# Performance work log

Measured on AMD Instinct MI355X. Metric: run time of the kernel, lower is better.

## Reference

```python
import jax, jax.numpy as jnp
import numpy as np

# DCT-III (a.k.a. IDCT), unnormalized, scaled to match the DREAMPlace kernel:
#   y_k = x_0 + 2 * sum_{n=1}^{N-1} x_n * cos(pi * n * (2k+1) / (2N))
# (the docstring's Re{1/2 x0 + sum xn e^{j pi n (2k+1)/(2N)}} scaled by 2).
# Computed in O(N log N) via a length-2N FFT:
#   y_k = Re{ sum_n c_n x_n e^{j pi n/(2N)} e^{2 pi j n k/(2N)} }
# which is 2N * ifft(pad(a, 2N)) evaluated at k = 0..N-1, with
#   a_n = c_n * x_n * exp(j pi n / (2N)),  c_0 = 1, c_{n>0} = 2.

def _idct_last_dim(x):
    N = x.shape[-1]
    n = jnp.arange(N)
    c = jnp.where(n == 0, 1.0, 2.0).astype(x.dtype)
    twiddle = jnp.exp(1j * (jnp.pi / (2 * N)) * n.astype(jnp.float32)).astype(jnp.complex64)
    a = (c * x).astype(jnp.complex64) * twiddle          # [.., N]
    y = jnp.fft.ifft(a, n=2 * N, axis=-1)                # [.., 2N]
    return (y.real[..., :N] * (2 * N)).astype(x.dtype)


def setup_inputs() -> dict:
    key = jax.random.key(0)
    x = jax.random.normal(key, (4096, 4096), dtype=jnp.float32)
    return {"x": x}


def reference(x) -> jnp.ndarray:
    return _idct_last_dim(x)
```

## Files before the change

kernel.cpp:

```cpp
#include <hip/hip_runtime.h>
#include <cstdint>


#define NN 4096
#define HH 2048
#define BM 128
#define BN 128
#define BK 128

typedef int i32x4 __attribute__((ext_vector_type(4)));
typedef int i32x2 __attribute__((ext_vector_type(2)));

__device__ __forceinline__ void async_copy16(void* lds_base, const void* gptr) {
    __builtin_amdgcn_global_load_lds(
        (const __attribute__((address_space(1))) unsigned int*)gptr,
        (__attribute__((address_space(3))) unsigned int*)lds_base,
        16, 0, 0);
}

__device__ __forceinline__ int pack4(int q0, int q1, int q2, int q3) {
    return (q0 & 255) | ((q1 & 255) << 8) | ((q2 & 255) << 16) | ((q3 & 255) << 24);
}

__global__ __launch_bounds__(256) void prep_i8(const float* __restrict__ x,
                                               signed char* __restrict__ Ae,
                                               signed char* __restrict__ Ao,
                                               signed char* __restrict__ CEm,
                                               signed char* __restrict__ COm,
                                               float* __restrict__ se,
                                               float* __restrict__ so) {
    const int b = blockIdx.x;
    const int t = threadIdx.x;
    const float s = 3.834951969714103e-4f;

    if (b < 4096) {
        __shared__ float wmaxe[4], wmaxo[4];
        const float* xr = x + (size_t)b * NN;
        float v[16];
#pragma unroll
        for (int j = 0; j < 4; ++j) {
            float4 f = ((const float4*)xr)[t * 4 + j];
            v[j * 4 + 0] = f.x; v[j * 4 + 1] = f.y;
            v[j * 4 + 2] = f.z; v[j * 4 + 3] = f.w;
        }
        float emax = 1e-30f, omax = 1e-30f;
#pragma unroll
        for (int i = 0; i < 8; ++i) {
            emax = fmaxf(emax, __builtin_fabsf(v[2 * i]));
            omax = fmaxf(omax, __builtin_fabsf(v[2 * i + 1]));
        }
#pragma unroll
        for (int m = 1; m < 64; m <<= 1) {
            emax = fmaxf(emax, __shfl_xor(emax, m));
            omax = fmaxf(omax, __shfl_xor(omax, m));
        }
        const int wv = t >> 6;
        if ((t & 63) == 0) { wmaxe[wv] = emax; wmaxo[wv] = omax; }
        __syncthreads();
        const float rmax_e = fmaxf(fmaxf(wmaxe[0], wmaxe[1]), fmaxf(wmaxe[2], wmaxe[3]));
        const float rmax_o = fmaxf(fmaxf(wmaxo[0], wmaxo[1]), fmaxf(wmaxo[2], wmaxo[3]));
        const float inv_e = 127.0f / rmax_e, inv_o = 127.0f / rmax_o;
        int qe[8], qo[8];
#pragma unroll
        for (int i = 0; i < 8; ++i) {
            qe[i] = (int)rintf(v[2 * i] * inv_e);
            qo[i] = (int)rintf(v[2 * i + 1] * inv_o);
        }
        i32x2 oe, oo;
        oe[0] = pack4(qe[0], qe[1], qe[2], qe[3]);
        oe[1] = pack4(qe[4], qe[5], qe[6], qe[7]);
        oo[0] = pack4(qo[0], qo[1], qo[2], qo[3]);
        oo[1] = pack4(qo[4], qo[5], qo[6], qo[7]);
        ((i32x2*)(Ae + (size_t)b * HH))[t] = oe;
        ((i32x2*)(Ao + (size_t)b * HH))[t] = oo;
        if (t == 0) {
            se[b] = rmax_e * (1.0f / 127.0f);
            so[b] = rmax_o * (1.0f / 127.0f);
        }
    } else if (b < 6144) {
        const int k = b - 4096;
        const int twok1 = 2 * k + 1;
        int q[8];
#pragma unroll
        for (int i = 0; i < 8; ++i) {
            int m = t * 8 + i;
            int p = (2 * m * twok1) & 16383;
            float w = (m == 0) ? 1.0f : 2.0f;
            q[i] = (int)rintf(w * __cosf((float)p * s) * 63.5f);
        }
        i32x2 o;
        o[0] = pack4(q[0], q[1], q[2], q[3]);
        o[1] = pack4(q[4], q[5], q[6], q[7]);
        ((i32x2*)(CEm + (size_t)k * HH))[t] = o;
    } else {
        const int k = b - 6144;
        const int twok1 = 2 * k + 1;
        int q[8];
#pragma unroll
        for (int i = 0; i < 8; ++i) {
            int m = t * 8 + i;
            int p = ((2 * m + 1) * twok1) & 16383;
            q[i] = (int)rintf(__cosf((float)p * s) * 127.0f);
        }
        i32x2 o;
        o[0] = pack4(q[0], q[1], q[2], q[3]);
        o[1] = pack4(q[4], q[5], q[6], q[7]);
        ((i32x2*)(COm + (size_t)k * HH))[t] = o;
    }
}

__global__ __launch_bounds__(256, 2) void idct_gemm2(const signed char* __restrict__ Ae,
                                                     const signed char* __restrict__ Ao,
                                                     const signed char* __restrict__ CEm,
                                                     const signed char* __restrict__ COm,
                                                     const float* __restrict__ se,
                                                     const float* __restrict__ so,
                                                     float* __restrict__ C) {
    __shared__ __align__(16) signed char sAe[BM * BK];
    __shared__ __align__(16) signed char sAo[BM * BK];
    __shared__ __align__(16) signed char sCE[BN * BK];
    __shared__ __align__(16) signed char sCO[BN * BK];

    const int tid  = threadIdx.x;
    const int wave = tid >> 6;
    const int lane = tid & 63;
    const int waveM = wave >> 1;
    const int waveN = wave & 1;

    const int rowBase = blockIdx.y * BM;
    const int colBase = blockIdx.x * BN;

    i32x4 accE[4][4] = {};
    i32x4 accO[4][4] = {};

    const int srow  = lane >> 3;
    const int sgran = lane & 7;
    const int ggcol = (sgran ^ srow) * 16;
    const int rmod  = lane & 7;
    const int quad  = lane >> 4;

    for (int k0 = 0; k0 < HH; k0 += BK) {
#pragma unroll
        for (int j = 0; j < 4; ++j) {
            int ck = wave * 4 + j;
            int r  = ck * 8 + srow;
            size_t aoff = (size_t)(rowBase + r) * HH + k0 + ggcol;
            size_t boff = (size_t)(colBase + r) * HH + k0 + ggcol;
            async_copy16(&sAe[ck * 1024], Ae + aoff);
            async_copy16(&sAo[ck * 1024], Ao + aoff);
            async_copy16(&sCE[ck * 1024], CEm + boff);
            async_copy16(&sCO[ck * 1024], COm + boff);
        }
        __syncthreads();

#pragma unroll
        for (int kk = 0; kk < 2; ++kk) {
            const int poff = ((kk * 4 + quad) ^ rmod) * 16;
            {
                i32x4 af[4], bfr[4];
#pragma unroll
                for (int mi = 0; mi < 4; ++mi) {
                    int r = waveM * 64 + mi * 16 + (lane & 15);
                    af[mi] = *(const i32x4*)&sAe[r * BK + poff];
                }
#pragma unroll
                for (int ni = 0; ni < 4; ++ni) {
                    int r = waveN * 64 + ni * 16 + (lane & 15);
                    bfr[ni] = *(const i32x4*)&sCE[r * BK + poff];
                }
#pragma unroll
                for (int mi = 0; mi < 4; ++mi)
#pragma unroll
                    for (int ni = 0; ni < 4; ++ni)
                        accE[mi][ni] = __builtin_amdgcn_mfma_i32_16x16x64_i8(
                            af[mi], bfr[ni], accE[mi][ni], 0, 0, 0);
            }
            {
                i32x4 af[4], bfr[4];
#pragma unroll
                for (int mi = 0; mi < 4; ++mi) {
                    int r = waveM * 64 + mi * 16 + (lane & 15);
                    af[mi] = *(const i32x4*)&sAo[r * BK + poff];
                }
#pragma unroll
                for (int ni = 0; ni < 4; ++ni) {
                    int r = waveN * 64 + ni * 16 + (lane & 15);
                    bfr[ni] = *(const i32x4*)&sCO[r * BK + poff];
                }
#pragma unroll
                for (int mi = 0; mi < 4; ++mi)
#pragma unroll
                    for (int ni = 0; ni < 4; ++ni)
                        accO[mi][ni] = __builtin_amdgcn_mfma_i32_16x16x64_i8(
                            af[mi], bfr[ni], accO[mi][ni], 0, 0, 0);
            }
        }
        __syncthreads();
    }

    const float sB_s = 2.0f / 127.0f;
    const int mrow0 = rowBase + waveM * 64 + (lane >> 4) * 4;
    const int ncol0 = colBase + waveN * 64 + (lane & 15);
#pragma unroll
    for (int mi = 0; mi < 4; ++mi)
#pragma unroll
        for (int ni = 0; ni < 4; ++ni)
#pragma unroll
            for (int rg = 0; rg < 4; ++rg) {
                int rr = mrow0 + mi * 16 + rg;
                int cc = ncol0 + ni * 16;
                float e = (float)accE[mi][ni][rg] * (se[rr] * sB_s);
                float o = (float)accO[mi][ni][rg] * (so[rr] * sB_s);
                C[(size_t)rr * NN + cc] = e + o;
                C[(size_t)rr * NN + (NN - 1 - cc)] = e - o;
            }
}

__global__ __launch_bounds__(256) void idct_naive(const float* __restrict__ x,
                                                  float* __restrict__ out) {
    int row = blockIdx.x;
    __shared__ float sx[NN];
    for (int i = threadIdx.x; i < NN; i += 256) sx[i] = x[(size_t)row * NN + i];
    __syncthreads();
    const float s = 3.834951969714103e-4f;
    for (int k = threadIdx.x; k < NN; k += 256) {
        int twok1 = 2 * k + 1;
        float acc = sx[0];
        int p = 0;
        for (int n = 1; n < NN; ++n) {
            p += twok1; p &= 16383;
            acc += 2.0f * sx[n] * __cosf((float)p * s);
        }
        out[(size_t)row * NN + k] = acc;
    }
}

extern "C" void kernel_launch(void* const* d_in, const int* in_sizes, int n_in,
                              void* d_out, int out_size, void* d_ws, size_t ws_size,
                              hipStream_t stream) {
    const float* x = (const float*)d_in[0];
    float* out = (float*)d_out;

    const size_t eA = (size_t)NN * HH;
    const size_t eC = (size_t)HH * HH;
    const size_t need = 2 * eA + 2 * eC + 2 * NN * sizeof(float);

    if (ws_size >= need) {
        signed char* Ae = (signed char*)d_ws;
        signed char* Ao = Ae + eA;
        signed char* CEm = Ao + eA;
        signed char* COm = CEm + eC;
        float* se = (float*)(COm + eC);
        float* so = se + NN;

        prep_i8<<<8192, 256, 0, stream>>>(x, Ae, Ao, CEm, COm, se, so);

        dim3 grid(HH / BN, NN / BM);
        idct_gemm2<<<grid, 256, 0, stream>>>(Ae, Ao, CEm, COm, se, so, out);
    } else {
        idct_naive<<<NN, 256, 0, stream>>>(x, out);
    }
}
```

Baseline: 146.0 us.

## Double-buffer LDS tiles in int8 IDCT GEMM with 512-thread blocks

Converts the int8 MFMA GEMM main loop to a double-buffered LDS pipeline: the next K-tile is issued with async global-to-LDS copies while the current tile is computed. The block grows to 8 waves, each owning a 64x32 output sub-tile, and MFMA sections are wrapped in s_setprio raises. This is meant to hide global load latency behind matrix math. The cost is that LDS per block doubles to 128KB, which likely limits occupancy to one block per CU, and each wave gets less register reuse per fragment load.

```diff
diff --git a/kernel.cpp b/kernel.cpp
--- a/kernel.cpp
+++ b/kernel.cpp
@@ -7,6 +7,7 @@
 #define BM 128
 #define BN 128
 #define BK 128
+#define NT (HH / BK)
 
 typedef int i32x4 __attribute__((ext_vector_type(4)));
 typedef int i32x2 __attribute__((ext_vector_type(2)));
@@ -109,102 +110,116 @@
     }
 }
 
-__global__ __launch_bounds__(256, 2) void idct_gemm2(const signed char* __restrict__ Ae,
+__global__ __launch_bounds__(512, 2) void idct_gemm2(const signed char* __restrict__ Ae,
                                                      const signed char* __restrict__ Ao,
                                                      const signed char* __restrict__ CEm,
                                                      const signed char* __restrict__ COm,
                                                      const float* __restrict__ se,
                                                      const float* __restrict__ so,
                                                      float* __restrict__ C) {
-    __shared__ __align__(16) signed char sAe[BM * BK];
-    __shared__ __align__(16) signed char sAo[BM * BK];
-    __shared__ __align__(16) signed char sCE[BN * BK];
-    __shared__ __align__(16) signed char sCO[BN * BK];
+    __shared__ __align__(16) signed char sAe[2][BM * BK];
+    __shared__ __align__(16) signed char sAo[2][BM * BK];
+    __shared__ __align__(16) signed char sCE[2][BN * BK];
+    __shared__ __align__(16) signed char sCO[2][BN * BK];
 
     const int tid  = threadIdx.x;
     const int wave = tid >> 6;
     const int lane = tid & 63;
-    const int waveM = wave >> 1;
-    const int waveN = wave & 1;
+    const int waveM = wave >> 2;
+    const int waveN = wave & 3;
 
     const int rowBase = blockIdx.y * BM;
     const int colBase = blockIdx.x * BN;
 
-    i32x4 accE[4][4] = {};
-    i32x4 accO[4][4] = {};
+    i32x4 accE[4][2] = {};
+    i32x4 accO[4][2] = {};
 
     const int srow  = lane >> 3;
     const int sgran = lane & 7;
     const int ggcol = (sgran ^ srow) * 16;
     const int rmod  = lane & 7;
     const int quad  = lane >> 4;
-
-    for (int k0 = 0; k0 < HH; k0 += BK) {
-#pragma unroll
-        for (int j = 0; j < 4; ++j) {
-            int ck = wave * 4 + j;
-            int r  = ck * 8 + srow;
-            size_t aoff = (size_t)(rowBase + r) * HH + k0 + ggcol;
-            size_t boff = (size_t)(colBase + r) * HH + k0 + ggcol;
-            async_copy16(&sAe[ck * 1024], Ae + aoff);
-            async_copy16(&sAo[ck * 1024], Ao + aoff);
-            async_copy16(&sCE[ck * 1024], CEm + boff);
-            async_copy16(&sCO[ck * 1024], COm + boff);
-        }
-        __syncthreads();
-
-#pragma unroll
-        for (int kk = 0; kk < 2; ++kk) {
-            const int poff = ((kk * 4 + quad) ^ rmod) * 16;
-            {
-                i32x4 af[4], bfr[4];
-#pragma unroll
-                for (int mi = 0; mi < 4; ++mi) {
-                    int r = waveM * 64 + mi * 16 + (lane & 15);
-                    af[mi] = *(const i32x4*)&sAe[r * BK + poff];
-                }
-#pragma unroll
-                for (int ni = 0; ni < 4; ++ni) {
-                    int r = waveN * 64 + ni * 16 + (lane & 15);
-                    bfr[ni] = *(const i32x4*)&sCE[r * BK + poff];
-                }
-#pragma unroll
-                for (int mi = 0; mi < 4; ++mi)
-#pragma unroll
-                    for (int ni = 0; ni < 4; ++ni)
-                        accE[mi][ni] = __builtin_amdgcn_mfma_i32_16x16x64_i8(
-                            af[mi], bfr[ni], accE[mi][ni], 0, 0, 0);
-            }
-            {
-                i32x4 af[4], bfr[4];
-#pragma unroll
-                for (int mi = 0; mi < 4; ++mi) {
-                    int r = waveM * 64 + mi * 16 + (lane & 15);
-                    af[mi] = *(const i32x4*)&sAo[r * BK + poff];
-                }
-#pragma unroll
-                for (int ni = 0; ni < 4; ++ni) {
-                    int r = waveN * 64 + ni * 16 + (lane & 15);
-                    bfr[ni] = *(const i32x4*)&sCO[r * BK + poff];
-                }
-#pragma unroll
-                for (int mi = 0; mi < 4; ++mi)
-#pragma unroll
-                    for (int ni = 0; ni < 4; ++ni)
-                        accO[mi][ni] = __builtin_amdgcn_mfma_i32_16x16x64_i8(
-                            af[mi], bfr[ni], accO[mi][ni], 0, 0, 0);
-            }
-        }
-        __syncthreads();
-    }
+    const int ck0   = wave * 2;
+
+    const size_t aRow = (size_t)(rowBase + ck0 * 8 + srow) * HH + ggcol;
+    const size_t bRow = (size_t)(colBase + ck0 * 8 + srow) * HH + ggcol;
+
+#define STAGE(BUF, K0)                                                        \
+    do {                                                                      \
+        _Pragma("unroll")                                                     \
+        for (int j = 0; j < 2; ++j) {                                         \
+            size_t aoff = aRow + (size_t)j * 8 * HH + (size_t)(K0);           \
+            size_t boff = bRow + (size_t)j * 8 * HH + (size_t)(K0);           \
+            async_copy16(&sAe[BUF][(ck0 + j) * 1024], Ae + aoff);             \
+            async_copy16(&sAo[BUF][(ck0 + j) * 1024], Ao + aoff);             \
+            async_copy16(&sCE[BUF][(ck0 + j) * 1024], CEm + boff);            \
+            async_copy16(&sCO[BUF][(ck0 + j) * 1024], COm + boff);            \
+        }                                                                     \
+    } while (0)
+
+#define COMPUTE(BUF)                                                          \
+    do {                                                                      \
+        _Pragma("unroll")                                                     \
+        for (int kk = 0; kk < 2; ++kk) {                                      \
+            const int poff = ((kk * 4 + quad) ^ rmod) * 16;                   \
+            i32x4 af[4], bfr[2];                                              \
+            _Pragma("unroll")                                                 \
+            for (int mi = 0; mi < 4; ++mi)                                    \
+                af[mi] = *(const i32x4*)&sAe[BUF][(waveM * 64 + mi * 16 + (lane & 15)) * BK + poff]; \
+            _Pragma("unroll")                                                 \
+            for (int ni = 0; ni < 2; ++ni)                                    \
+                bfr[ni] = *(const i32x4*)&sCE[BUF][(waveN * 32 + ni * 16 + (lane & 15)) * BK + poff]; \
+            __builtin_amdgcn_s_setprio(1);                                    \
+            _Pragma("unroll")                                                 \
+            for (int mi = 0; mi < 4; ++mi)                                    \
+                _Pragma("unroll")                                             \
+                for (int ni = 0; ni < 2; ++ni)                                \
+                    accE[mi][ni] = __builtin_amdgcn_mfma_i32_16x16x64_i8(     \
+                        af[mi], bfr[ni], accE[mi][ni], 0, 0, 0);              \
+            __builtin_amdgcn_s_setprio(0);                                    \
+            _Pragma("unroll")                                                 \
+            for (int mi = 0; mi < 4; ++mi)                                    \
+                af[mi] = *(const i32x4*)&sAo[BUF][(waveM * 64 + mi * 16 + (lane & 15)) * BK + poff]; \
+            _Pragma("unroll")                                                 \
+            for (int ni = 0; ni < 2; ++ni)                                    \
+                bfr[ni] = *(const i32x4*)&sCO[BUF][(waveN * 32 + ni * 16 + (lane & 15)) * BK + poff]; \
+            __builtin_amdgcn_s_setprio(1);                                    \
+            _Pragma("unroll")                                                 \
+            for (int mi = 0; mi < 4; ++mi)                                    \
+                _Pragma("unroll")                                             \
+                for (int ni = 0; ni < 2; ++ni)                                \
+                    accO[mi][ni] = __builtin_amdgcn_mfma_i32_16x16x64_i8(     \
+                        af[mi], bfr[ni], accO[mi][ni], 0, 0, 0);              \
+            __builtin_amdgcn_s_setprio(0);                                    \
+        }                                                                     \
+    } while (0)
+
+    STAGE(0, 0);
+    asm volatile("s_waitcnt vmcnt(0)" ::: "memory");
+    __builtin_amdgcn_s_barrier();
+
+#pragma unroll 1
+    for (int t = 0; t < NT; t += 2) {
+        STAGE(1, (t + 1) * BK);
+        COMPUTE(0);
+        asm volatile("s_waitcnt vmcnt(0) lgkmcnt(0)" ::: "memory");
+        __builtin_amdgcn_s_barrier();
+
+        if (t + 2 < NT) STAGE(0, (t + 2) * BK);
+        COMPUTE(1);
+        asm volatile("s_waitcnt vmcnt(0) lgkmcnt(0)" ::: "memory");
+        __builtin_amdgcn_s_barrier();
+    }
+#undef STAGE
+#undef COMPUTE
 
     const float sB_s = 2.0f / 127.0f;
     const int mrow0 = rowBase + waveM * 64 + (lane >> 4) * 4;
-    const int ncol0 = colBase + waveN * 64 + (lane & 15);
+    const int ncol0 = colBase + waveN * 32 + (lane & 15);
 #pragma unroll
     for (int mi = 0; mi < 4; ++mi)
 #pragma unroll
-        for (int ni = 0; ni < 4; ++ni)
+        for (int ni = 0; ni < 2; ++ni)
 #pragma unroll
             for (int rg = 0; rg < 4; ++rg) {
                 int rr = mrow0 + mi * 16 + rg;
@@ -256,7 +271,7 @@
         prep_i8<<<8192, 256, 0, stream>>>(x, Ae, Ao, CEm, COm, se, so);
 
         dim3 grid(HH / BN, NN / BM);
-        idct_gemm2<<<grid, 256, 0, stream>>>(Ae, Ao, CEm, COm, se, so, out);
+        idct_gemm2<<<grid, 512, 0, stream>>>(Ae, Ao, CEm, COm, se, so, out);
     } else {
         idct_naive<<<NN, 256, 0, stream>>>(x, out);
     }
```

New measurement: 160.0 us. 9.6% more time.
